# Kernel tuning notes

Measured on AMD Instinct MI355X. Metric: run time of the kernel, lower is better.

Reference implementation:

```python
import jax, jax.numpy as jnp
import numpy as np

N_NODES = 100000
N_EDGES = 600000
N_FEAT = 128
HIDDEN = 128
N_CLASSES = 40  # output dim = num_classes + 1 = 41


def setup_inputs() -> dict:
    key = jax.random.key(0)
    k = jax.random.split(key, 6)
    x = jax.random.normal(k[0], (N_NODES, N_FEAT), dtype=jnp.float32)
    edge_index = jax.random.randint(k[1], (2, N_EDGES), 0, N_NODES, dtype=jnp.int64)
    # GCNConv params (Glorot-ish scale)
    W1 = jax.random.normal(k[2], (N_FEAT, HIDDEN), dtype=jnp.float32) / np.sqrt(N_FEAT)
    b1 = jnp.zeros((HIDDEN,), dtype=jnp.float32)
    W2 = jax.random.normal(k[3], (HIDDEN, N_CLASSES + 1), dtype=jnp.float32) / np.sqrt(HIDDEN)
    b2 = jnp.zeros((N_CLASSES + 1,), dtype=jnp.float32)
    return {"x": x, "W1": W1, "b1": b1, "W2": W2, "b2": b2, "edge_index": edge_index}


def _gcn_layer(x, W, b, src, dst, norm, n):
    # linear transform then normalized scatter-add aggregation (PyG GCNConv)
    h = x @ W                                  # [N, out]
    msg = h[src] * norm[:, None]               # gather + per-edge normalization
    out = jax.ops.segment_sum(msg, dst, num_segments=n)
    return out + b


def reference(x, W1, b1, W2, b2, edge_index):
    n = x.shape[0]
    # add self-loops
    loops = jnp.arange(n, dtype=edge_index.dtype)
    src = jnp.concatenate([edge_index[0], loops])
    dst = jnp.concatenate([edge_index[1], loops])
    # symmetric degree normalization: D^{-1/2} A_hat D^{-1/2}
    deg = jax.ops.segment_sum(jnp.ones_like(dst, dtype=x.dtype), dst, num_segments=n)
    dinv = jnp.where(deg > 0, jax.lax.rsqrt(deg), 0.0)
    norm = dinv[src] * dinv[dst]               # [E + N]
    h = _gcn_layer(x, W1, b1, src, dst, norm, n)
    h = jax.nn.relu(h)
    # dropout is identity in eval mode
    h = _gcn_layer(h, W2, b2, src, dst, norm, n)
    return jax.nn.log_softmax(h, axis=1)
```

## Files before the change

kernel.cpp:

```cpp
#include <hip/hip_runtime.h>
#include <math.h>

#define N_NODES 100000
#define N_EDGES 600000
#define NC 41
#define CAP 32
#define BLDB 2048

typedef __attribute__((ext_vector_type(8))) short bf16x8;
typedef __attribute__((ext_vector_type(8))) unsigned short u16x8;
typedef __attribute__((ext_vector_type(4))) float f32x4;

static __device__ __forceinline__ unsigned short f2b(float f) {
    unsigned u = __float_as_uint(f);
    unsigned r = ((u >> 16) & 1u) + 0x7fffu;
    return (unsigned short)((u + r) >> 16);
}
static __device__ __forceinline__ float b2f(unsigned short s) {
    return __uint_as_float(((unsigned)s) << 16);
}
static __device__ __forceinline__ u16x8 zero8() {
    u16x8 z;
#pragma unroll
    for (int i = 0; i < 8; ++i) z[i] = 0;
    return z;
}

__global__ __launch_bounds__(256) void k_build(const float* __restrict__ x,
                                               unsigned short* __restrict__ xb,
                                               const int* __restrict__ src,
                                               const int* __restrict__ dst,
                                               int* __restrict__ cnt,
                                               int* __restrict__ eidx) {
    int tid = blockIdx.x * 256 + threadIdx.x;
    const int nthr = BLDB * 256;
    for (int i = tid; i < N_NODES * 16; i += nthr) {
        float4 lo = ((const float4*)x)[i * 2];
        float4 hi = ((const float4*)x)[i * 2 + 1];
        u16x8 o;
        o[0] = f2b(lo.x); o[1] = f2b(lo.y); o[2] = f2b(lo.z); o[3] = f2b(lo.w);
        o[4] = f2b(hi.x); o[5] = f2b(hi.y); o[6] = f2b(hi.z); o[7] = f2b(hi.w);
        ((u16x8*)xb)[i] = o;
    }
    for (int e = tid; e < N_EDGES; e += nthr) {
        int s = src[e];
        int d = dst[e];
        int pos = atomicAdd(&cnt[d], 1);
        if (pos < CAP) eidx[(size_t)d * CAP + pos] = s;
    }
}

__global__ __launch_bounds__(256, 8) void k_aggx(const unsigned short* __restrict__ xb,
                                                 const int* __restrict__ cnt,
                                                 const int* __restrict__ eidx,
                                                 unsigned short* __restrict__ R) {
    int tid = threadIdx.x;
    int node = blockIdx.x * 16 + (tid >> 4);
    int j = tid & 15;
    int deg = min(cnt[node], CAP);
    float di = rsqrtf((float)(deg + 1));
    float acc[8];
    {
        u16x8 v = *(const u16x8*)(xb + (size_t)node * 128 + j * 8);
#pragma unroll
        for (int i = 0; i < 8; ++i) acc[i] = b2f(v[i]) * di;
    }
    const int* ebase = eidx + (size_t)node * CAP;
    int e = 0;
    int s0 = (0 < deg) ? ebase[0] : -1;
    int s1 = (1 < deg) ? ebase[1] : -1;
    u16x8 r0 = zero8(), r1 = zero8();
    int c0 = 0, c1 = 0;
    if (s0 >= 0) { r0 = *(const u16x8*)(xb + (size_t)s0 * 128 + j * 8); c0 = cnt[s0]; }
    if (s1 >= 0) { r1 = *(const u16x8*)(xb + (size_t)s1 * 128 + j * 8); c1 = cnt[s1]; }
    while (s0 >= 0) {
        int s2 = (e + 2 < deg) ? ebase[e + 2] : -1;
        u16x8 r2 = zero8();
        int c2 = 0;
        if (s2 >= 0) { r2 = *(const u16x8*)(xb + (size_t)s2 * 128 + j * 8); c2 = cnt[s2]; }
        float w = rsqrtf((float)(c0 + 1));
#pragma unroll
        for (int i = 0; i < 8; ++i) acc[i] = fmaf(b2f(r0[i]), w, acc[i]);
        s0 = s1; s1 = s2; c0 = c1; c1 = c2; r0 = r1; r1 = r2; ++e;
    }
    u16x8 o;
#pragma unroll
    for (int i = 0; i < 8; ++i) o[i] = f2b(acc[i] * di);
    *(u16x8*)(R + (size_t)node * 128 + j * 8) = o;
}

__global__ __launch_bounds__(512) void k_mm(const unsigned short* __restrict__ R,
                                            const float* __restrict__ W1,
                                            const float* __restrict__ b1,
                                            const float* __restrict__ W2,
                                            const int* __restrict__ cnt,
                                            unsigned short* __restrict__ h2) {
    __shared__ unsigned short Wt1[128 * 132];
    __shared__ unsigned short Wt2[48 * 132];
    __shared__ unsigned short rows[32 * 136];
    int tid = threadIdx.x;
    for (int i = tid; i < 128 * 128; i += 512) {
        int k = i >> 7, n = i & 127;
        Wt1[n * 132 + k] = f2b(W1[i]);
    }
    for (int i = tid; i < 128 * 48; i += 512) {
        int k = i / 48, n = i % 48;
        Wt2[n * 132 + k] = f2b((n < NC) ? W2[k * NC + n] : 0.f);
    }
    __syncthreads();

    int l = tid & 63, w = tid >> 6;
    int lr = l & 15, g = l >> 4;
    int rh = w >> 2;
    int cg = w & 3;
    int rh2 = w / 3, ct = w % 3;

    bf16x8 f1[2][4];
#pragma unroll
    for (int c = 0; c < 2; ++c) {
        int n = (cg * 2 + c) * 16 + lr;
#pragma unroll
        for (int kt = 0; kt < 4; ++kt) {
            const unsigned short* p = &Wt1[n * 132 + kt * 32 + g * 4];
            short4 lo = *(const short4*)p;
            short4 hi = *(const short4*)(p + 16);
            bf16x8 f;
            f[0] = lo.x; f[1] = lo.y; f[2] = lo.z; f[3] = lo.w;
            f[4] = hi.x; f[5] = hi.y; f[6] = hi.z; f[7] = hi.w;
            f1[c][kt] = f;
        }
    }
    bf16x8 f2[4];
    if (w < 6) {
#pragma unroll
        for (int kt = 0; kt < 4; ++kt) {
            const unsigned short* p = &Wt2[(ct * 16 + lr) * 132 + kt * 32 + g * 4];
            short4 lo = *(const short4*)p;
            short4 hi = *(const short4*)(p + 16);
            bf16x8 f;
            f[0] = lo.x; f[1] = lo.y; f[2] = lo.z; f[3] = lo.w;
            f[4] = hi.x; f[5] = hi.y; f[6] = hi.z; f[7] = hi.w;
            f2[kt] = f;
        }
    }
    float bia0 = b1[(cg * 2) * 16 + lr];
    float bia1 = b1[(cg * 2 + 1) * 16 + lr];

    int srow = tid >> 4, scol = tid & 15;
    for (int t = blockIdx.x; t < N_NODES / 32; t += gridDim.x) {
        *(u16x8*)&rows[srow * 136 + scol * 8] =
            *(const u16x8*)(R + ((size_t)t * 32 + srow) * 128 + scol * 8);
        __syncthreads();

        f32x4 a0 = {0.f, 0.f, 0.f, 0.f};
        f32x4 a1 = {0.f, 0.f, 0.f, 0.f};
#pragma unroll
        for (int kt = 0; kt < 4; ++kt) {
            const unsigned short* pa = &rows[(rh * 16 + lr) * 136 + kt * 32 + g * 4];
            short4 alo = *(const short4*)pa;
            short4 ahi = *(const short4*)(pa + 16);
            bf16x8 a;
            a[0] = alo.x; a[1] = alo.y; a[2] = alo.z; a[3] = alo.w;
            a[4] = ahi.x; a[5] = ahi.y; a[6] = ahi.z; a[7] = ahi.w;
            a0 = __builtin_amdgcn_mfma_f32_16x16x32_bf16(a, f1[0][kt], a0, 0, 0, 0);
            a1 = __builtin_amdgcn_mfma_f32_16x16x32_bf16(a, f1[1][kt], a1, 0, 0, 0);
        }
        __syncthreads();

#pragma unroll
        for (int i = 0; i < 4; ++i) {
            int row = rh * 16 + g * 4 + i;
            rows[row * 136 + (cg * 2) * 16 + lr]     = f2b(fmaxf(a0[i] + bia0, 0.f));
            rows[row * 136 + (cg * 2 + 1) * 16 + lr] = f2b(fmaxf(a1[i] + bia1, 0.f));
        }
        __syncthreads();

        if (w < 6) {
            f32x4 c0 = {0.f, 0.f, 0.f, 0.f};
#pragma unroll
            for (int kt = 0; kt < 4; ++kt) {
                const unsigned short* pa = &rows[(rh2 * 16 + lr) * 136 + kt * 32 + g * 4];
                short4 alo = *(const short4*)pa;
                short4 ahi = *(const short4*)(pa + 16);
                bf16x8 a;
                a[0] = alo.x; a[1] = alo.y; a[2] = alo.z; a[3] = alo.w;
                a[4] = ahi.x; a[5] = ahi.y; a[6] = ahi.z; a[7] = ahi.w;
                c0 = __builtin_amdgcn_mfma_f32_16x16x32_bf16(a, f2[kt], c0, 0, 0, 0);
            }
#pragma unroll
            for (int i = 0; i < 4; ++i) {
                int row = t * 32 + rh2 * 16 + g * 4 + i;
                float dv = rsqrtf((float)(min(cnt[row], CAP) + 1));
                h2[(size_t)row * 48 + ct * 16 + lr] = f2b(c0[i] * dv);
            }
        }
        __syncthreads();
    }
}

__global__ __launch_bounds__(256, 8) void k_gather2(const unsigned short* __restrict__ h2,
                                                    float* __restrict__ out,
                                                    const int* __restrict__ cnt,
                                                    const int* __restrict__ eidx,
                                                    const float* __restrict__ b2) {
    __shared__ float so[8 * NC + 8];
    int tid = threadIdx.x;
    int nloc = tid >> 5;
    int node = blockIdx.x * 8 + nloc;
    int l = tid & 31;
    int g = l >> 3, j = l & 7;
    bool act = (j < 6);
    int deg = min(cnt[node], CAP);
    float di = rsqrtf((float)(deg + 1));
    float acc[8];
#pragma unroll
    for (int i = 0; i < 8; ++i) acc[i] = 0.f;
    if (g == 0 && act) {
        u16x8 v = *(const u16x8*)(h2 + (size_t)node * 48 + j * 8);
#pragma unroll
        for (int i = 0; i < 8; ++i) acc[i] = b2f(v[i]);
    }
    const int* ebase = eidx + (size_t)node * CAP;
    int e = g;
    int s0 = (e < deg) ? ebase[e] : -1;
    int s1 = (e + 4 < deg) ? ebase[e + 4] : -1;
    u16x8 r0 = zero8(), r1 = zero8();
    if (s0 >= 0 && act) r0 = *(const u16x8*)(h2 + (size_t)s0 * 48 + j * 8);
    if (s1 >= 0 && act) r1 = *(const u16x8*)(h2 + (size_t)s1 * 48 + j * 8);
    while (s0 >= 0) {
        int s2 = (e + 8 < deg) ? ebase[e + 8] : -1;
        u16x8 r2 = zero8();
        if (s2 >= 0 && act) r2 = *(const u16x8*)(h2 + (size_t)s2 * 48 + j * 8);
#pragma unroll
        for (int i = 0; i < 8; ++i) acc[i] += b2f(r0[i]);
        s0 = s1; s1 = s2; r0 = r1; r1 = r2; e += 4;
    }
#pragma unroll
    for (int i = 0; i < 8; ++i) acc[i] += __shfl_xor(acc[i], 8);
#pragma unroll
    for (int i = 0; i < 8; ++i) acc[i] += __shfl_xor(acc[i], 16);
    int c0 = j * 8;
    float vv[8];
#pragma unroll
    for (int i = 0; i < 8; ++i)
        vv[i] = (act && c0 + i < NC) ? acc[i] * di + b2[c0 + i] : -INFINITY;
    float m = vv[0];
#pragma unroll
    for (int i = 1; i < 8; ++i) m = fmaxf(m, vv[i]);
#pragma unroll
    for (int o = 4; o; o >>= 1) m = fmaxf(m, __shfl_xor(m, o));
    float sm = 0.f;
#pragma unroll
    for (int i = 0; i < 8; ++i) sm += (act && c0 + i < NC) ? expf(vv[i] - m) : 0.f;
#pragma unroll
    for (int o = 4; o; o >>= 1) sm += __shfl_xor(sm, o);
    float lg = logf(sm);
    if (g == 0 && act) {
#pragma unroll
        for (int i = 0; i < 8; ++i) {
            int c = c0 + i;
            if (c < NC) so[nloc * NC + c] = vv[i] - m - lg;
        }
    }
    __syncthreads();
    float4* ob = (float4*)(out + (size_t)blockIdx.x * (8 * NC));
    const float4* sb = (const float4*)so;
    if (tid < 2 * NC) ob[tid] = sb[tid];
}

extern "C" void kernel_launch(void* const* d_in, const int* in_sizes, int n_in,
                              void* d_out, int out_size, void* d_ws, size_t ws_size,
                              hipStream_t stream) {
    const float* x  = (const float*)d_in[0];
    const float* W1 = (const float*)d_in[1];
    const float* b1 = (const float*)d_in[2];
    const float* W2 = (const float*)d_in[3];
    const float* b2 = (const float*)d_in[4];
    const int*   ei = (const int*)d_in[5];
    const int* src = ei;
    const int* dst = ei + N_EDGES;
    float* out = (float*)d_out;

    char* ws = (char*)d_ws;
    int* cnt  = (int*)ws;
    int* eidx = (int*)(ws + (1u << 20));
    unsigned short* xb = (unsigned short*)(ws + (15u << 20));
    unsigned short* R  = (unsigned short*)(ws + (41u << 20));
    unsigned short* h2 = (unsigned short*)(ws + (67u << 20));

    hipMemsetAsync(cnt, 0, N_NODES * sizeof(int), stream);
    k_build<<<BLDB, 256, 0, stream>>>(x, xb, src, dst, cnt, eidx);

    k_aggx<<<N_NODES / 16, 256, 0, stream>>>(xb, cnt, eidx, R);
    k_mm<<<1024, 512, 0, stream>>>(R, W1, b1, W2, cnt, h2);

    k_gather2<<<N_NODES / 8, 256, 0, stream>>>(h2, out, cnt, eidx, b2);
}
```

Before: 153.1 us.

## Fuse first-layer aggregation into the matmul kernel and interleave build loops

Merges the neighbour aggregation kernel into the MFMA matmul kernel, so each 32-node tile is aggregated directly into shared memory instead of being written to and re-read from a global R buffer. It also interleaves the edge bucketing and bf16 conversion loops in the build kernel so their latencies can overlap. This removes one launch and a round trip of the intermediate through global memory. In exchange, the gather latency now sits inside a kernel with heavy register use and only 1024 blocks of 512 threads, so there may be less occupancy available to hide the irregular gathers.

```diff
diff --git a/kernel.cpp b/kernel.cpp
--- a/kernel.cpp
+++ b/kernel.cpp
@@ -6,6 +6,7 @@
 #define NC 41
 #define CAP 32
 #define BLDB 2048
+#define NT32 (N_NODES / 32)
 
 typedef __attribute__((ext_vector_type(8))) short bf16x8;
 typedef __attribute__((ext_vector_type(8))) unsigned short u16x8;
@@ -34,67 +35,35 @@
                                                int* __restrict__ eidx) {
     int tid = blockIdx.x * 256 + threadIdx.x;
     const int nthr = BLDB * 256;
-    for (int i = tid; i < N_NODES * 16; i += nthr) {
-        float4 lo = ((const float4*)x)[i * 2];
-        float4 hi = ((const float4*)x)[i * 2 + 1];
-        u16x8 o;
-        o[0] = f2b(lo.x); o[1] = f2b(lo.y); o[2] = f2b(lo.z); o[3] = f2b(lo.w);
-        o[4] = f2b(hi.x); o[5] = f2b(hi.y); o[6] = f2b(hi.z); o[7] = f2b(hi.w);
-        ((u16x8*)xb)[i] = o;
-    }
-    for (int e = tid; e < N_EDGES; e += nthr) {
-        int s = src[e];
-        int d = dst[e];
-        int pos = atomicAdd(&cnt[d], 1);
-        if (pos < CAP) eidx[(size_t)d * CAP + pos] = s;
-    }
-}
-
-__global__ __launch_bounds__(256, 8) void k_aggx(const unsigned short* __restrict__ xb,
-                                                 const int* __restrict__ cnt,
-                                                 const int* __restrict__ eidx,
-                                                 unsigned short* __restrict__ R) {
-    int tid = threadIdx.x;
-    int node = blockIdx.x * 16 + (tid >> 4);
-    int j = tid & 15;
-    int deg = min(cnt[node], CAP);
-    float di = rsqrtf((float)(deg + 1));
-    float acc[8];
-    {
-        u16x8 v = *(const u16x8*)(xb + (size_t)node * 128 + j * 8);
-#pragma unroll
-        for (int i = 0; i < 8; ++i) acc[i] = b2f(v[i]) * di;
-    }
-    const int* ebase = eidx + (size_t)node * CAP;
-    int e = 0;
-    int s0 = (0 < deg) ? ebase[0] : -1;
-    int s1 = (1 < deg) ? ebase[1] : -1;
-    u16x8 r0 = zero8(), r1 = zero8();
-    int c0 = 0, c1 = 0;
-    if (s0 >= 0) { r0 = *(const u16x8*)(xb + (size_t)s0 * 128 + j * 8); c0 = cnt[s0]; }
-    if (s1 >= 0) { r1 = *(const u16x8*)(xb + (size_t)s1 * 128 + j * 8); c1 = cnt[s1]; }
-    while (s0 >= 0) {
-        int s2 = (e + 2 < deg) ? ebase[e + 2] : -1;
-        u16x8 r2 = zero8();
-        int c2 = 0;
-        if (s2 >= 0) { r2 = *(const u16x8*)(xb + (size_t)s2 * 128 + j * 8); c2 = cnt[s2]; }
-        float w = rsqrtf((float)(c0 + 1));
-#pragma unroll
-        for (int i = 0; i < 8; ++i) acc[i] = fmaf(b2f(r0[i]), w, acc[i]);
-        s0 = s1; s1 = s2; c0 = c1; c1 = c2; r0 = r1; r1 = r2; ++e;
-    }
-    u16x8 o;
-#pragma unroll
-    for (int i = 0; i < 8; ++i) o[i] = f2b(acc[i] * di);
-    *(u16x8*)(R + (size_t)node * 128 + j * 8) = o;
-}
-
-__global__ __launch_bounds__(512) void k_mm(const unsigned short* __restrict__ R,
-                                            const float* __restrict__ W1,
-                                            const float* __restrict__ b1,
-                                            const float* __restrict__ W2,
-                                            const int* __restrict__ cnt,
-                                            unsigned short* __restrict__ h2) {
+    const int convN = N_NODES * 16;
+    int i = tid, e = tid;
+    while (i < convN || e < N_EDGES) {
+        if (e < N_EDGES) {
+            int s = src[e];
+            int d = dst[e];
+            int pos = atomicAdd(&cnt[d], 1);
+            if (pos < CAP) eidx[(size_t)d * CAP + pos] = s;
+            e += nthr;
+        }
+        if (i < convN) {
+            float4 lo = ((const float4*)x)[i * 2];
+            float4 hi = ((const float4*)x)[i * 2 + 1];
+            u16x8 o;
+            o[0] = f2b(lo.x); o[1] = f2b(lo.y); o[2] = f2b(lo.z); o[3] = f2b(lo.w);
+            o[4] = f2b(hi.x); o[5] = f2b(hi.y); o[6] = f2b(hi.z); o[7] = f2b(hi.w);
+            ((u16x8*)xb)[i] = o;
+            i += nthr;
+        }
+    }
+}
+
+__global__ __launch_bounds__(512) void k_aggmm(const unsigned short* __restrict__ xb,
+                                               const int* __restrict__ cnt,
+                                               const int* __restrict__ eidx,
+                                               const float* __restrict__ W1,
+                                               const float* __restrict__ b1,
+                                               const float* __restrict__ W2,
+                                               unsigned short* __restrict__ h2) {
     __shared__ unsigned short Wt1[128 * 132];
     __shared__ unsigned short Wt2[48 * 132];
     __shared__ unsigned short rows[32 * 136];
@@ -114,6 +83,7 @@
     int rh = w >> 2;
     int cg = w & 3;
     int rh2 = w / 3, ct = w % 3;
+    int grp = tid >> 4, j = tid & 15;
 
     bf16x8 f1[2][4];
 #pragma unroll
@@ -146,10 +116,38 @@
     float bia0 = b1[(cg * 2) * 16 + lr];
     float bia1 = b1[(cg * 2 + 1) * 16 + lr];
 
-    int srow = tid >> 4, scol = tid & 15;
-    for (int t = blockIdx.x; t < N_NODES / 32; t += gridDim.x) {
-        *(u16x8*)&rows[srow * 136 + scol * 8] =
-            *(const u16x8*)(R + ((size_t)t * 32 + srow) * 128 + scol * 8);
+    for (int t = blockIdx.x; t < NT32; t += gridDim.x) {
+        {
+            int node = t * 32 + grp;
+            int deg = min(cnt[node], CAP);
+            float di = rsqrtf((float)(deg + 1));
+            float acc[8];
+            u16x8 v = *(const u16x8*)(xb + (size_t)node * 128 + j * 8);
+#pragma unroll
+            for (int i = 0; i < 8; ++i) acc[i] = b2f(v[i]) * di;
+            const int* ebase = eidx + (size_t)node * CAP;
+            int e = 0;
+            int s0 = (0 < deg) ? ebase[0] : -1;
+            int s1 = (1 < deg) ? ebase[1] : -1;
+            u16x8 r0 = zero8(), r1 = zero8();
+            int c0 = 0, c1 = 0;
+            if (s0 >= 0) { r0 = *(const u16x8*)(xb + (size_t)s0 * 128 + j * 8); c0 = cnt[s0]; }
+            if (s1 >= 0) { r1 = *(const u16x8*)(xb + (size_t)s1 * 128 + j * 8); c1 = cnt[s1]; }
+            while (s0 >= 0) {
+                int s2 = (e + 2 < deg) ? ebase[e + 2] : -1;
+                u16x8 r2 = zero8();
+                int c2 = 0;
+                if (s2 >= 0) { r2 = *(const u16x8*)(xb + (size_t)s2 * 128 + j * 8); c2 = cnt[s2]; }
+                float wgt = rsqrtf((float)(c0 + 1));
+#pragma unroll
+                for (int i = 0; i < 8; ++i) acc[i] = fmaf(b2f(r0[i]), wgt, acc[i]);
+                s0 = s1; s1 = s2; c0 = c1; c1 = c2; r0 = r1; r1 = r2; ++e;
+            }
+            u16x8 o;
+#pragma unroll
+            for (int i = 0; i < 8; ++i) o[i] = f2b(acc[i] * di);
+            *(u16x8*)&rows[grp * 136 + j * 8] = o;
+        }
         __syncthreads();
 
         f32x4 a0 = {0.f, 0.f, 0.f, 0.f};
@@ -285,14 +283,12 @@
     int* cnt  = (int*)ws;
     int* eidx = (int*)(ws + (1u << 20));
     unsigned short* xb = (unsigned short*)(ws + (15u << 20));
-    unsigned short* R  = (unsigned short*)(ws + (41u << 20));
-    unsigned short* h2 = (unsigned short*)(ws + (67u << 20));
+    unsigned short* h2 = (unsigned short*)(ws + (41u << 20));
 
     hipMemsetAsync(cnt, 0, N_NODES * sizeof(int), stream);
     k_build<<<BLDB, 256, 0, stream>>>(x, xb, src, dst, cnt, eidx);
 
-    k_aggx<<<N_NODES / 16, 256, 0, stream>>>(xb, cnt, eidx, R);
-    k_mm<<<1024, 512, 0, stream>>>(R, W1, b1, W2, cnt, h2);
+    k_aggmm<<<1024, 512, 0, stream>>>(xb, cnt, eidx, W1, b1, W2, h2);
 
     k_gather2<<<N_NODES / 8, 256, 0, stream>>>(h2, out, cnt, eidx, b2);
 }
```

Measured after the change: 163.7 us. 6.9% more time.
